# Performance work log

Hardware: AMD Instinct MI355X
Metric: run time of the kernel (lower is better)

The kernel has to match this reference:

```python
import jax, jax.numpy as jnp
import numpy as np


def setup_inputs() -> dict:
    key = jax.random.key(0)
    k1, k2 = jax.random.split(key)
    N, D = 65536, 512
    feeds = jax.random.normal(k1, (N, D), dtype=jnp.float32)
    feeds_repeat_times = jax.random.randint(k2, (N,), 0, 8)
    return {
        "feeds": feeds,
        "feeds_repeat_times": feeds_repeat_times,
        "output_feeds_size": 262144,
    }


def reference(feeds, feeds_repeat_times, output_feeds_size):
    # Equivalent of the per-row repeat + cat + pad + truncate, as one fused gather.
    # Output row j comes from source row i where cumsum(repeats) first exceeds j.
    cum = jnp.cumsum(feeds_repeat_times)          # [N]
    total = cum[-1]                               # total repeated rows
    pos = jnp.arange(output_feeds_size)           # [S]
    idx = jnp.searchsorted(cum, pos, side="right")  # source row per output row
    valid = pos < total                           # rows beyond total are zero pad
    idx = jnp.clip(idx, 0, feeds.shape[0] - 1)
    out = jnp.where(valid[:, None], feeds[idx], jnp.zeros((), dtype=feeds.dtype))
    return out
```

## Files before the change

### kernel.cpp

```cpp
#include <hip/hip_runtime.h>

#define NROWS 65536
#define DCOLS 512
#define D4    128

typedef float f32x4 __attribute__((ext_vector_type(4)));

__global__ __launch_bounds__(1024) void scan_kernel(const int* __restrict__ rep,
                                                    int* __restrict__ cum) {
    __shared__ int sdata[1024];
    const int t = threadIdx.x;
    const int base = t * 64;

    int4 v[16];
    const int4* rep4 = (const int4*)(rep + base);
#pragma unroll
    for (int k = 0; k < 16; ++k) v[k] = rep4[k];

    int partial = 0;
#pragma unroll
    for (int k = 0; k < 16; ++k) partial += v[k].x + v[k].y + v[k].z + v[k].w;

    sdata[t] = partial;
    __syncthreads();
    for (int off = 1; off < 1024; off <<= 1) {
        int add = (t >= off) ? sdata[t - off] : 0;
        __syncthreads();
        sdata[t] += add;
        __syncthreads();
    }
    int running = sdata[t] - partial;

    int4* cum4 = (int4*)(cum + base);
#pragma unroll
    for (int k = 0; k < 16; ++k) {
        int4 x;
        running += v[k].x; x.x = running;
        running += v[k].y; x.y = running;
        running += v[k].z; x.z = running;
        running += v[k].w; x.w = running;
        cum4[k] = x;
    }
}

__global__ __launch_bounds__(256) void expand_kernel(const f32x4* __restrict__ feeds,
                                                     const int* __restrict__ rep,
                                                     const int* __restrict__ cum,
                                                     f32x4* __restrict__ out,
                                                     int S) {
    const int wave = (int)((blockIdx.x * blockDim.x + threadIdx.x) >> 6);
    const int lane = threadIdx.x & 63;

    const int i     = wave;
    const int end   = cum[i];
    const int r     = rep[i];
    const int start = end - r;
    const int stop  = end < S ? end : S;

    if (start < stop) {
        const f32x4* src = feeds + (long long)i * D4;
        const f32x4 a = src[lane];
        const f32x4 b = src[lane + 64];
        for (int j = start; j < stop; ++j) {
            f32x4* dst = out + (long long)j * D4;
            dst[lane]      = a;
            dst[lane + 64] = b;
        }
    }

    const int total = cum[NROWS - 1];
    const f32x4 z = (f32x4)0.f;
    for (int j = total + wave; j < S; j += NROWS) {
        f32x4* dst = out + (long long)j * D4;
        dst[lane]      = z;
        dst[lane + 64] = z;
    }
}

extern "C" void kernel_launch(void* const* d_in, const int* in_sizes, int n_in,
                              void* d_out, int out_size, void* d_ws, size_t ws_size,
                              hipStream_t stream) {
    const float* feeds = (const float*)d_in[0];
    const int*   rep   = (const int*)d_in[1];
    const int S = out_size / DCOLS;

    int* cum = (int*)d_ws;

    scan_kernel<<<1, 1024, 0, stream>>>(rep, cum);
    expand_kernel<<<NROWS / 4, 256, 0, stream>>>((const f32x4*)feeds, rep, cum,
                                                 (f32x4*)d_out, S);
}
```

Measured before the change: 630.4 us.

## Replace per-source expand with multi-block scan, index build, and per-output gather

Replaces the single-block scan and source-row-driven expand with four kernels: a chunked reduce-then-scan, a kernel that writes a 16-bit source index for each output row, and a gather kernel in which each wave produces four output rows. The goal is to remove the serialized single-block scan and the load imbalance where waves with many repeats loop over stores while others sit idle. The gather also remaps block IDs across eight groups, likely aimed at the XCDs. In exchange it adds launches, an index-buffer round trip, and it rereads source rows once per output row instead of once per source row.

```diff
diff --git a/kernel.cpp b/kernel.cpp
--- a/kernel.cpp
+++ b/kernel.cpp
@@ -3,77 +3,102 @@
 #define NROWS 65536
 #define DCOLS 512
 #define D4    128
+#define CHUNK 256
+#define NCHUNK (NROWS / CHUNK)
 
 typedef float f32x4 __attribute__((ext_vector_type(4)));
 
-__global__ __launch_bounds__(1024) void scan_kernel(const int* __restrict__ rep,
-                                                    int* __restrict__ cum) {
-    __shared__ int sdata[1024];
+
+__global__ __launch_bounds__(256) void chunk_sum_kernel(const int* __restrict__ rep,
+                                                        int* __restrict__ chunksum) {
+    const int b = blockIdx.x;
     const int t = threadIdx.x;
-    const int base = t * 64;
+    int v = rep[b * CHUNK + t];
+#pragma unroll
+    for (int off = 32; off; off >>= 1) v += __shfl_down(v, off);
+    __shared__ int ws4[4];
+    if ((t & 63) == 0) ws4[t >> 6] = v;
+    __syncthreads();
+    if (t == 0) chunksum[b] = ws4[0] + ws4[1] + ws4[2] + ws4[3];
+}
 
-    int4 v[16];
-    const int4* rep4 = (const int4*)(rep + base);
-#pragma unroll
-    for (int k = 0; k < 16; ++k) v[k] = rep4[k];
-
-    int partial = 0;
-#pragma unroll
-    for (int k = 0; k < 16; ++k) partial += v[k].x + v[k].y + v[k].z + v[k].w;
-
-    sdata[t] = partial;
+__global__ __launch_bounds__(256) void scan_chunks_kernel(const int* __restrict__ chunksum,
+                                                          int* __restrict__ chunkoff,
+                                                          int* __restrict__ totalp) {
+    __shared__ int s[NCHUNK];
+    const int t = threadIdx.x;
+    const int v = chunksum[t];
+    s[t] = v;
     __syncthreads();
-    for (int off = 1; off < 1024; off <<= 1) {
-        int add = (t >= off) ? sdata[t - off] : 0;
+    for (int off = 1; off < NCHUNK; off <<= 1) {
+        int add = (t >= off) ? s[t - off] : 0;
         __syncthreads();
-        sdata[t] += add;
+        s[t] += add;
         __syncthreads();
     }
-    int running = sdata[t] - partial;
-
-    int4* cum4 = (int4*)(cum + base);
-#pragma unroll
-    for (int k = 0; k < 16; ++k) {
-        int4 x;
-        running += v[k].x; x.x = running;
-        running += v[k].y; x.y = running;
-        running += v[k].z; x.z = running;
-        running += v[k].w; x.w = running;
-        cum4[k] = x;
-    }
+    chunkoff[t] = s[t] - v;
+    if (t == NCHUNK - 1) totalp[0] = s[t];
 }
 
-__global__ __launch_bounds__(256) void expand_kernel(const f32x4* __restrict__ feeds,
-                                                     const int* __restrict__ rep,
-                                                     const int* __restrict__ cum,
+__global__ __launch_bounds__(256) void build_idx_kernel(const int* __restrict__ rep,
+                                                        const int* __restrict__ chunkoff,
+                                                        unsigned short* __restrict__ idx16,
+                                                        int S) {
+    const int b = blockIdx.x;
+    const int t = threadIdx.x;
+    const int i = b * CHUNK + t;
+    const int r = rep[i];
+    __shared__ int s[CHUNK];
+    s[t] = r;
+    __syncthreads();
+    for (int off = 1; off < CHUNK; off <<= 1) {
+        int add = (t >= off) ? s[t - off] : 0;
+        __syncthreads();
+        s[t] += add;
+        __syncthreads();
+    }
+    int end = chunkoff[b] + s[t];
+    const int start = end - r;
+    if (start >= S) return;
+    if (end > S) end = S;
+    for (int j = start; j < end; ++j) idx16[j] = (unsigned short)i;
+}
+
+__global__ __launch_bounds__(256) void gather_kernel(const f32x4* __restrict__ feeds,
+                                                     const unsigned short* __restrict__ idx16,
+                                                     const int* __restrict__ totalp,
                                                      f32x4* __restrict__ out,
                                                      int S) {
-    const int wave = (int)((blockIdx.x * blockDim.x + threadIdx.x) >> 6);
+    int bid = blockIdx.x;
+    const int cpx = gridDim.x >> 3;
+    bid = (bid & 7) * cpx + (bid >> 3);
+
+    const int wave = bid * 4 + (threadIdx.x >> 6);
     const int lane = threadIdx.x & 63;
+    const int j0 = wave * 4;
+    if (j0 >= S) return;
 
-    const int i     = wave;
-    const int end   = cum[i];
-    const int r     = rep[i];
-    const int start = end - r;
-    const int stop  = end < S ? end : S;
+    const int total = totalp[0];
 
-    if (start < stop) {
-        const f32x4* src = feeds + (long long)i * D4;
-        const f32x4 a = src[lane];
-        const f32x4 b = src[lane + 64];
-        for (int j = start; j < stop; ++j) {
-            f32x4* dst = out + (long long)j * D4;
-            dst[lane]      = a;
-            dst[lane + 64] = b;
+    f32x4 a[4], b[4];
+#pragma unroll
+    for (int q = 0; q < 4; ++q) {
+        const int j = j0 + q;
+        if (j < total) {
+            const int si = idx16[j];
+            const f32x4* src = feeds + (long long)si * D4;
+            a[q] = src[lane];
+            b[q] = src[lane + 64];
+        } else {
+            a[q] = (f32x4)0.f;
+            b[q] = (f32x4)0.f;
         }
     }
-
-    const int total = cum[NROWS - 1];
-    const f32x4 z = (f32x4)0.f;
-    for (int j = total + wave; j < S; j += NROWS) {
-        f32x4* dst = out + (long long)j * D4;
-        dst[lane]      = z;
-        dst[lane + 64] = z;
+#pragma unroll
+    for (int q = 0; q < 4; ++q) {
+        f32x4* dst = out + (long long)(j0 + q) * D4;
+        dst[lane]      = a[q];
+        dst[lane + 64] = b[q];
     }
 }
 
@@ -84,9 +109,15 @@
     const int*   rep   = (const int*)d_in[1];
     const int S = out_size / DCOLS;
 
-    int* cum = (int*)d_ws;
+    int* ws       = (int*)d_ws;
+    int* chunksum = ws;
+    int* chunkoff = ws + 256;
+    int* totalp   = ws + 512;
+    unsigned short* idx16 = (unsigned short*)(ws + 1024);
 
-    scan_kernel<<<1, 1024, 0, stream>>>(rep, cum);
-    expand_kernel<<<NROWS / 4, 256, 0, stream>>>((const f32x4*)feeds, rep, cum,
-                                                 (f32x4*)d_out, S);
+    chunk_sum_kernel<<<NCHUNK, CHUNK, 0, stream>>>(rep, chunksum);
+    scan_chunks_kernel<<<1, NCHUNK, 0, stream>>>(chunksum, chunkoff, totalp);
+    build_idx_kernel<<<NCHUNK, CHUNK, 0, stream>>>(rep, chunkoff, idx16, S);
+    gather_kernel<<<S / 16, 256, 0, stream>>>((const f32x4*)feeds, idx16, totalp,
+                                              (f32x4*)d_out, S);
 }
```

Measured after the change: 620.4 us. Within noise of the previous version (-1.6%).
